# Kernel tuning notes

Hardware: AMD Instinct MI355X
Metric: run time of the kernel (lower is better)

Reference implementation:

```python
import jax, jax.numpy as jnp
import numpy as np

# Llama-7B FFN up-proj quantized with HQQ 4-bit, group_size=64, axis=0
OUT, IN, GS = 11008, 4096, 64
G = OUT * IN // GS  # 704512 groups


def setup_inputs() -> dict:
    key = jax.random.key(0)
    k1, k2, k3, k4, k5 = jax.random.split(key, 5)
    # packed 4-bit weights: two nibbles per byte, shape [GS//2, G]
    W_q = jax.random.randint(k1, (GS // 2, G), 0, 256, dtype=jnp.int32)
    # per-group scale (meta['scale'] = 1/scale from quantize) and zero
    scale = jax.random.uniform(k2, (1, G), jnp.float32, minval=1e-3, maxval=1e-2)
    zero = jax.random.uniform(k3, (1, G), jnp.float32, minval=0.0, maxval=15.0)
    # decode-style activations: 8 sequences, 1 token each
    x = jax.random.normal(k4, (8, 1, IN), dtype=jnp.float32)
    bias = jax.random.normal(k5, (OUT,), dtype=jnp.float32) * 0.01
    return {"W_q": W_q, "scale": scale, "zero": zero, "x": x, "bias": bias}


def reference(W_q, scale, zero, x, bias):
    # BitPack.unpack_4bit_u8: high nibble rows stacked on low nibble rows
    hi = (W_q >> 4) & 0xF
    lo = W_q & 0xF
    W_q_p = jnp.concatenate([hi, lo], axis=0).astype(x.dtype)  # [GS, G]
    # Quantizer.dequantize: (W_q_p - zero) * scale, reshape to weight shape
    W_r = ((W_q_p - zero) * scale).reshape(OUT, IN)  # [out, in]
    # torch.nn.functional.linear(x, W_r, bias)
    return jnp.einsum('bsi,oi->bso', x, W_r) + bias
```

## Files before the change

### kernel.cpp

```cpp
#include <hip/hip_runtime.h>


#define OUT_ 11008
#define IN_ 4096
#define G_ 704512
#define OC_ 172
#define KS 4
#define KC (IN_ / KS)
#define ITERS (KC / 256)
#define SIB (OC_ * KS)
#define NB (4 * SIB)

typedef const __attribute__((address_space(1))) void* gptr1_t;
typedef __attribute__((address_space(3))) void* sptr3_t;

__device__ __forceinline__ void gload_lds16(const float* g, float* l) {
    __builtin_amdgcn_global_load_lds((gptr1_t)g, (sptr3_t)l, 16, 0, 0);
}

__global__ __launch_bounds__(256, 4)
void hqq_gemv(const int* __restrict__ Wq, const float* __restrict__ scale,
              const float* __restrict__ zero, const float* __restrict__ x,
              float* __restrict__ ws) {
    __shared__ float x_lds[8 * KC];
    __shared__ float s_lds[KC];
    __shared__ float z_lds[KC];

    const int lane = threadIdx.x;
    const int ty   = threadIdx.y;
    const int tid  = ty * 64 + lane;
    const int bid  = blockIdx.x;
    const int bx   = bid / SIB;
    const int rem  = bid % SIB;
    const int oc   = rem >> 2;
    const int ks   = rem & 3;
    const int rq0  = bx * 8 + ty * 2;

    const int kbase = ks * KC;
    const int gb = oc * IN_ + kbase;

    const int wf = ty * 256;
    gload_lds16(scale + gb + wf + lane * 4, s_lds + wf);
    gload_lds16(zero  + gb + wf + lane * 4, z_lds + wf);
#pragma unroll
    for (int r = 0; r < 8; ++r) {
        gload_lds16(x + r * IN_ + kbase + wf + lane * 4, x_lds + r * 1024 + wf);
    }

    asm volatile("" ::: "memory");

    const int* __restrict__ wqA = Wq + (long)rq0 * G_ + gb;
    const int* __restrict__ wqB = wqA + G_;
    int4 qA[ITERS], qB[ITERS];
#pragma unroll
    for (int it = 0; it < ITERS; ++it) {
        qA[it] = *(const int4*)(wqA + it * 256 + lane * 4);
        qB[it] = *(const int4*)(wqB + it * 256 + lane * 4);
    }

    asm volatile("s_waitcnt vmcnt(8)\n\ts_barrier" ::: "memory");

    float acc[4][8];
#pragma unroll
    for (int r = 0; r < 4; ++r)
#pragma unroll
        for (int b = 0; b < 8; ++b) acc[r][b] = 0.f;

#pragma unroll
    for (int it = 0; it < ITERS; ++it) {
        const int i = it * 256 + lane * 4;
        const float4 s4 = *(const float4*)(s_lds + i);
        const float4 z4 = *(const float4*)(z_lds + i);
        const float ss[4] = {s4.x, s4.y, s4.z, s4.w};
        const float zs[4] = {-z4.x * s4.x, -z4.y * s4.y, -z4.z * s4.z, -z4.w * s4.w};
        const int qsA[4] = {qA[it].x, qA[it].y, qA[it].z, qA[it].w};
        const int qsB[4] = {qB[it].x, qB[it].y, qB[it].z, qB[it].w};

        float w[4][4];
#pragma unroll
        for (int j = 0; j < 4; ++j) {
            w[0][j] = fmaf((float)((qsA[j] >> 4) & 0xF), ss[j], zs[j]);
            w[1][j] = fmaf((float)( qsA[j]       & 0xF), ss[j], zs[j]);
            w[2][j] = fmaf((float)((qsB[j] >> 4) & 0xF), ss[j], zs[j]);
            w[3][j] = fmaf((float)( qsB[j]       & 0xF), ss[j], zs[j]);
        }
#pragma unroll
        for (int b = 0; b < 8; ++b) {
            const float4 xb = *(const float4*)(x_lds + b * KC + i);
#pragma unroll
            for (int r = 0; r < 4; ++r) {
                float a = acc[r][b];
                a = fmaf(xb.x, w[r][0], a);
                a = fmaf(xb.y, w[r][1], a);
                a = fmaf(xb.z, w[r][2], a);
                a = fmaf(xb.w, w[r][3], a);
                acc[r][b] = a;
            }
        }
    }

    float* red = x_lds;
    __syncthreads();
    const int obase = ty * 32;
#pragma unroll
    for (int r = 0; r < 4; ++r)
#pragma unroll
        for (int b = 0; b < 8; ++b) {
            const int o = obase + r * 8 + b;
            red[o * 64 + (lane ^ ((o & 7) << 2))] = acc[r][b];
        }
    __syncthreads();

    if (tid < 128) {
        const int o = tid;
        const int c = (o & 7) << 2;
        float s = 0.f;
#pragma unroll
        for (int j = 0; j < 16; ++j) {
            const float4 v = *(const float4*)(red + o * 64 + ((j * 4) ^ c));
            s += (v.x + v.y) + (v.z + v.w);
        }
        ws[(long)((bx * OC_ + oc) * KS + ks) * 128 + o] = s;
    }
}

__global__ void hqq_reduce(const float* __restrict__ ws,
                           const float* __restrict__ bias,
                           float* __restrict__ out) {
    const int t = blockIdx.x * 256 + threadIdx.x;
    if (t >= (NB / KS) * 128) return;
    const int c = t >> 7;
    const int o = t & 127;
    float v = 0.f;
#pragma unroll
    for (int k = 0; k < KS; ++k) v += ws[(c << 9) + (k << 7) + o];
    const int bx = c / OC_;
    const int oc = c % OC_;
    const int w_ = o >> 5;
    const int r  = (o >> 3) & 3;
    const int b  = o & 7;
    const int rq  = bx * 8 + w_ * 2 + (r >> 1);
    const int row = rq + ((r & 1) ? 32 : 0);
    const int oo  = row * OC_ + oc;
    out[b * OUT_ + oo] = v + bias[oo];
}

extern "C" void kernel_launch(void* const* d_in, const int* in_sizes, int n_in,
                              void* d_out, int out_size, void* d_ws, size_t ws_size,
                              hipStream_t stream) {
    const int*   Wq    = (const int*)d_in[0];
    const float* scale = (const float*)d_in[1];
    const float* zero  = (const float*)d_in[2];
    const float* x     = (const float*)d_in[3];
    const float* bias  = (const float*)d_in[4];
    float* out = (float*)d_out;
    float* ws  = (float*)d_ws;

    dim3 grid(NB);
    dim3 block(64, 4);
    hqq_gemv<<<grid, block, 0, stream>>>(Wq, scale, zero, x, ws);
    hqq_reduce<<<((NB / KS) * 128 + 255) / 256, 256, 0, stream>>>(ws, bias, out);
}
```

Before: 145.2 us.

## Process two output chunks per block with register prefetch and XCD-aware block mapping

Each block now handles two consecutive output-column chunks. It prefetches the second chunk's packed weights into registers while computing the first, which halves the grid size and reuses the x tile loaded into LDS. Scale and zero are now read straight from global memory instead of being staged in LDS. The cross-wave LDS reduction is replaced by a per-wave reduction using LDS plus shuffles, which removes __syncthreads. Block indices are remapped so consecutive work lands on the same XCD. Costs are higher register pressure from holding two weight buffers and fewer blocks to hide latency.

```diff
diff --git a/kernel.cpp b/kernel.cpp
--- a/kernel.cpp
+++ b/kernel.cpp
@@ -8,8 +8,9 @@
 #define KS 4
 #define KC (IN_ / KS)
 #define ITERS (KC / 256)
-#define SIB (OC_ * KS)
-#define NB (4 * SIB)
+#define STEPS 2
+#define NCHUNK (OC_ * KS)
+#define NB (NCHUNK * 4 / STEPS)
 
 typedef const __attribute__((address_space(1))) void* gptr1_t;
 typedef __attribute__((address_space(3))) void* sptr3_t;
@@ -23,104 +24,108 @@
               const float* __restrict__ zero, const float* __restrict__ x,
               float* __restrict__ ws) {
     __shared__ float x_lds[8 * KC];
-    __shared__ float s_lds[KC];
-    __shared__ float z_lds[KC];
+    __shared__ float red_lds[4 * 512];
 
     const int lane = threadIdx.x;
     const int ty   = threadIdx.y;
-    const int tid  = ty * 64 + lane;
     const int bid  = blockIdx.x;
-    const int bx   = bid / SIB;
-    const int rem  = bid % SIB;
-    const int oc   = rem >> 2;
-    const int ks   = rem & 3;
+    const int xcd  = bid & 7;
+    const int t    = xcd * (NB / 8) + (bid >> 3);
+    const int bx   = t & 3;
+    const int ks   = (t >> 2) & 3;
+    const int ocg  = t >> 4;
     const int rq0  = bx * 8 + ty * 2;
 
     const int kbase = ks * KC;
-    const int gb = oc * IN_ + kbase;
 
-    const int wf = ty * 256;
-    gload_lds16(scale + gb + wf + lane * 4, s_lds + wf);
-    gload_lds16(zero  + gb + wf + lane * 4, z_lds + wf);
 #pragma unroll
-    for (int r = 0; r < 8; ++r) {
-        gload_lds16(x + r * IN_ + kbase + wf + lane * 4, x_lds + r * 1024 + wf);
-    }
-
+    for (int r = 0; r < 8; ++r)
+        gload_lds16(x + r * IN_ + kbase + ty * 256 + lane * 4,
+                    x_lds + r * KC + ty * 256);
     asm volatile("" ::: "memory");
 
-    const int* __restrict__ wqA = Wq + (long)rq0 * G_ + gb;
+    const int* __restrict__ wqA = Wq + (long)rq0 * G_ +
+                                  (ocg * STEPS) * IN_ + kbase + lane * 4;
     const int* __restrict__ wqB = wqA + G_;
-    int4 qA[ITERS], qB[ITERS];
+    int4 qa[STEPS][ITERS], qb[STEPS][ITERS];
 #pragma unroll
     for (int it = 0; it < ITERS; ++it) {
-        qA[it] = *(const int4*)(wqA + it * 256 + lane * 4);
-        qB[it] = *(const int4*)(wqB + it * 256 + lane * 4);
+        qa[0][it] = *(const int4*)(wqA + it * 256);
+        qb[0][it] = *(const int4*)(wqB + it * 256);
     }
-
     asm volatile("s_waitcnt vmcnt(8)\n\ts_barrier" ::: "memory");
 
-    float acc[4][8];
-#pragma unroll
-    for (int r = 0; r < 4; ++r)
-#pragma unroll
-        for (int b = 0; b < 8; ++b) acc[r][b] = 0.f;
+    float* const red = red_lds + ty * 512;
 
 #pragma unroll
-    for (int it = 0; it < ITERS; ++it) {
-        const int i = it * 256 + lane * 4;
-        const float4 s4 = *(const float4*)(s_lds + i);
-        const float4 z4 = *(const float4*)(z_lds + i);
-        const float ss[4] = {s4.x, s4.y, s4.z, s4.w};
-        const float zs[4] = {-z4.x * s4.x, -z4.y * s4.y, -z4.z * s4.z, -z4.w * s4.w};
-        const int qsA[4] = {qA[it].x, qA[it].y, qA[it].z, qA[it].w};
-        const int qsB[4] = {qB[it].x, qB[it].y, qB[it].z, qB[it].w};
-
-        float w[4][4];
+    for (int s = 0; s < STEPS; ++s) {
+        if (s + 1 < STEPS) {
 #pragma unroll
-        for (int j = 0; j < 4; ++j) {
-            w[0][j] = fmaf((float)((qsA[j] >> 4) & 0xF), ss[j], zs[j]);
-            w[1][j] = fmaf((float)( qsA[j]       & 0xF), ss[j], zs[j]);
-            w[2][j] = fmaf((float)((qsB[j] >> 4) & 0xF), ss[j], zs[j]);
-            w[3][j] = fmaf((float)( qsB[j]       & 0xF), ss[j], zs[j]);
-        }
-#pragma unroll
-        for (int b = 0; b < 8; ++b) {
-            const float4 xb = *(const float4*)(x_lds + b * KC + i);
-#pragma unroll
-            for (int r = 0; r < 4; ++r) {
-                float a = acc[r][b];
-                a = fmaf(xb.x, w[r][0], a);
-                a = fmaf(xb.y, w[r][1], a);
-                a = fmaf(xb.z, w[r][2], a);
-                a = fmaf(xb.w, w[r][3], a);
-                acc[r][b] = a;
+            for (int it = 0; it < ITERS; ++it) {
+                qa[s + 1][it] = *(const int4*)(wqA + (s + 1) * IN_ + it * 256);
+                qb[s + 1][it] = *(const int4*)(wqB + (s + 1) * IN_ + it * 256);
             }
         }
-    }
+        const int oc = ocg * STEPS + s;
+        const int gb = oc * IN_ + kbase;
 
-    float* red = x_lds;
-    __syncthreads();
-    const int obase = ty * 32;
+        float acc[4][8];
 #pragma unroll
-    for (int r = 0; r < 4; ++r)
+        for (int r = 0; r < 4; ++r)
 #pragma unroll
-        for (int b = 0; b < 8; ++b) {
-            const int o = obase + r * 8 + b;
-            red[o * 64 + (lane ^ ((o & 7) << 2))] = acc[r][b];
+            for (int b = 0; b < 8; ++b) acc[r][b] = 0.f;
+
+#pragma unroll
+        for (int it = 0; it < ITERS; ++it) {
+            const int i = it * 256 + lane * 4;
+            const float4 s4 = *(const float4*)(scale + gb + i);
+            const float4 z4 = *(const float4*)(zero + gb + i);
+            const float ss[4] = {s4.x, s4.y, s4.z, s4.w};
+            const float zs[4] = {-z4.x * s4.x, -z4.y * s4.y,
+                                 -z4.z * s4.z, -z4.w * s4.w};
+            const int qsA[4] = {qa[s][it].x, qa[s][it].y, qa[s][it].z, qa[s][it].w};
+            const int qsB[4] = {qb[s][it].x, qb[s][it].y, qb[s][it].z, qb[s][it].w};
+
+            float w[4][4];
+#pragma unroll
+            for (int j = 0; j < 4; ++j) {
+                w[0][j] = fmaf((float)((qsA[j] >> 4) & 0xF), ss[j], zs[j]);
+                w[1][j] = fmaf((float)( qsA[j]       & 0xF), ss[j], zs[j]);
+                w[2][j] = fmaf((float)((qsB[j] >> 4) & 0xF), ss[j], zs[j]);
+                w[3][j] = fmaf((float)( qsB[j]       & 0xF), ss[j], zs[j]);
+            }
+#pragma unroll
+            for (int b = 0; b < 8; ++b) {
+                const float4 xb = *(const float4*)(x_lds + b * KC + i);
+#pragma unroll
+                for (int r = 0; r < 4; ++r) {
+                    float a = acc[r][b];
+                    a = fmaf(xb.x, w[r][0], a);
+                    a = fmaf(xb.y, w[r][1], a);
+                    a = fmaf(xb.z, w[r][2], a);
+                    a = fmaf(xb.w, w[r][3], a);
+                    acc[r][b] = a;
+                }
+            }
         }
-    __syncthreads();
 
-    if (tid < 128) {
-        const int o = tid;
-        const int c = (o & 7) << 2;
-        float s = 0.f;
 #pragma unroll
-        for (int j = 0; j < 16; ++j) {
-            const float4 v = *(const float4*)(red + o * 64 + ((j * 4) ^ c));
-            s += (v.x + v.y) + (v.z + v.w);
+        for (int m = 0; m < 4; ++m) {
+#pragma unroll
+            for (int b = 0; b < 8; ++b)
+                red[b * 64 + (lane ^ (b << 2))] = acc[m][b];
+            const int ro = lane >> 3;
+            const int c0 = (lane & 7) * 8;
+            const float4 u0 = *(const float4*)(red + ro * 64 + ((c0    ) ^ (ro << 2)));
+            const float4 u1 = *(const float4*)(red + ro * 64 + ((c0 + 4) ^ (ro << 2)));
+            float v = ((u0.x + u0.y) + (u0.z + u0.w)) +
+                      ((u1.x + u1.y) + (u1.z + u1.w));
+            v += __shfl_xor(v, 1, 64);
+            v += __shfl_xor(v, 2, 64);
+            v += __shfl_xor(v, 4, 64);
+            if ((lane & 7) == 0)
+                ws[(((bx * OC_ + oc) * KS + ks) << 7) + ty * 32 + m * 8 + ro] = v;
         }
-        ws[(long)((bx * OC_ + oc) * KS + ks) * 128 + o] = s;
     }
 }
 
@@ -128,7 +133,7 @@
                            const float* __restrict__ bias,
                            float* __restrict__ out) {
     const int t = blockIdx.x * 256 + threadIdx.x;
-    if (t >= (NB / KS) * 128) return;
+    if (t >= NCHUNK * 128) return;
     const int c = t >> 7;
     const int o = t & 127;
     float v = 0.f;
@@ -159,5 +164,5 @@
     dim3 grid(NB);
     dim3 block(64, 4);
     hqq_gemv<<<grid, block, 0, stream>>>(Wq, scale, zero, x, ws);
-    hqq_reduce<<<((NB / KS) * 128 + 255) / 256, 256, 0, stream>>>(ws, bias, out);
+    hqq_reduce<<<(NCHUNK * 128 + 255) / 256, 256, 0, stream>>>(ws, bias, out);
 }
```

New measurement: 389.2 us. 2.68x slower.
